# Kernel tuning notes

Measured on AMD Instinct MI355X. Metric: run time of the kernel, lower is better.

The kernel has to match this reference:

```python
import jax, jax.numpy as jnp
import numpy as np

N, E, D, H, C = 50000, 800000, 256, 8, 32  # C = D // H
STEPS = 6
NEG = 0.2  # leaky_relu negative slope (PyG HEATConv default)
ETD, EAD = 10, 50  # edge_type_emb_dim, edge_attr_emb_dim


def setup_inputs() -> dict:
    key = jax.random.key(0)
    ks = jax.random.split(key, 20)
    def g(k, shape, scale=0.05):
        return jax.random.normal(k, shape, dtype=jnp.float32) * scale
    return {
        "x": jax.random.normal(ks[0], (N, D), dtype=jnp.float32),
        "edge_index": jax.random.randint(ks[1], (2, E), 0, N),
        "edge_attr": jax.random.normal(ks[2], (E,), dtype=jnp.float32),
        "node_type": jax.random.randint(ks[3], (N,), 0, 2),
        "link_type": jax.random.randint(ks[4], (E,), 0, 3),
        # HEATConv params (shared across all 6 steps)
        "Wh": g(ks[5], (2, D, C)),          # HeteroLinear weight per node type
        "bh": g(ks[6], (2, C)),             # HeteroLinear bias per node type
        "Et": g(ks[7], (3, ETD)),           # edge type embedding table
        "Wea": g(ks[8], (1, EAD)),          # edge attr embedding (Linear, no bias)
        "Watt": g(ks[9], (2 * C + ETD + EAD, H)),  # attention (Linear, no bias)
        "Wlin": g(ks[10], (C + EAD, C)),    # message lin (Linear, no bias)
        # per-step FFN + LayerNorm params
        "ffn_w1": g(ks[11], (STEPS, D, 4 * D)),
        "ffn_b1": g(ks[12], (STEPS, 4 * D)),
        "ffn_w2": g(ks[13], (STEPS, 4 * D, D)),
        "ffn_b2": g(ks[14], (STEPS, D)),
        "ln1_g": jnp.ones((STEPS, D), jnp.float32),
        "ln1_b": jnp.zeros((STEPS, D), jnp.float32),
        "ln2_g": jnp.ones((STEPS, D), jnp.float32),
        "ln2_b": jnp.zeros((STEPS, D), jnp.float32),
    }


def _leaky(v):
    return jax.nn.leaky_relu(v, NEG)


def _layer_norm(h, g, b, eps=1e-5):
    mu = h.mean(-1, keepdims=True)
    var = h.var(-1, keepdims=True)  # biased, matches torch LayerNorm
    return (h - mu) * jax.lax.rsqrt(var + eps) * g + b


def _heat_conv(m, src, dst, edge_attr, node_type, link_type, Wh, bh, Et, Wea, Watt, Wlin):
    # node-type-specific linear (HeteroLinear, 2 types): compute both, select
    x_all = jnp.einsum('nd,tdc->tnc', m, Wh) + bh[:, None, :]     # [2,N,C]
    x = jnp.where(node_type[:, None] == 0, x_all[0], x_all[1])    # [N,C]
    ete = _leaky(Et[link_type])                                   # [E,ETD]
    eae = _leaky(edge_attr[:, None] @ Wea)                        # [E,EAD]
    feat = jnp.concatenate([x[dst], x[src], ete, eae], axis=-1)   # [E, 2C+ETD+EAD]
    logits = _leaky(feat @ Watt)                                  # [E,H]
    # segment softmax over incoming edges of each destination node
    mx = jax.ops.segment_max(logits, dst, num_segments=N)
    e = jnp.exp(logits - mx[dst])
    s = jax.ops.segment_sum(e, dst, num_segments=N)
    alpha = e / (s[dst] + 1e-16)                                  # [E,H]
    msg = jnp.concatenate([x[src], eae], axis=-1) @ Wlin          # [E,C]
    per_edge = alpha[:, :, None] * msg[:, None, :]                # [E,H,C]
    out = jax.ops.segment_sum(per_edge, dst, num_segments=N)      # [N,H,C]
    return out.reshape(N, H * C)  # concat heads; root_weight=False


def reference(x, edge_index, edge_attr, node_type, link_type, Wh, bh, Et, Wea, Watt, Wlin,
              ffn_w1, ffn_b1, ffn_w2, ffn_b2, ln1_g, ln1_b, ln2_g, ln2_b):
    src, dst = edge_index[0], edge_index[1]
    m = x
    for i in range(STEPS):
        h = _heat_conv(m, src, dst, edge_attr, node_type, link_type,
                       Wh, bh, Et, Wea, Watt, Wlin)
        m = _layer_norm(h + m, ln1_g[i], ln1_b[i])
        f = jax.nn.relu(m @ ffn_w1[i] + ffn_b1[i]) @ ffn_w2[i] + ffn_b2[i]
        m = _layer_norm(f + m, ln2_g[i], ln2_b[i])
    return m
```

## Files before the change

kernel.cpp:

```cpp
#include <hip/hip_runtime.h>

#define Nn 50000
#define Ee 800000
#define STEPSn 6
#define NP 49

typedef _Float16 half8 __attribute__((ext_vector_type(8)));
typedef _Float16 half4v __attribute__((ext_vector_type(4)));
typedef float floatx4 __attribute__((ext_vector_type(4)));

typedef __attribute__((address_space(1))) void gvoid_t;
typedef __attribute__((address_space(3))) void svoid_t;

__device__ __forceinline__ float leakyf(float v) { return v > 0.f ? v : 0.2f * v; }

__device__ __forceinline__ void gload16(const void* g, void* l) {
    __builtin_amdgcn_global_load_lds((const gvoid_t*)g, (svoid_t*)l, 16, 0, 0);
}

template <int CTRL>
__device__ __forceinline__ float dppf(float v) {
    return __int_as_float(__builtin_amdgcn_update_dpp(
        0, __float_as_int(v), CTRL, 0xF, 0xF, true));
}

__global__ void k_count(const int* __restrict__ dst, int* __restrict__ cnt) {
    int e = blockIdx.x * 256 + threadIdx.x;
    if (e < Ee) atomicAdd(&cnt[dst[e]], 1);
}

__global__ __launch_bounds__(256) void k_scan1(const int* __restrict__ cnt,
                                               int* __restrict__ part) {
    int b = blockIdx.x, t = threadIdx.x;
    int s = 0;
#pragma unroll
    for (int j = 0; j < 4; ++j) {
        int idx = b * 1024 + j * 256 + t;
        if (idx < Nn) s += cnt[idx];
    }
#pragma unroll
    for (int d = 1; d < 64; d <<= 1) s += __shfl_xor(s, d);
    __shared__ int ws[4];
    if ((t & 63) == 0) ws[t >> 6] = s;
    __syncthreads();
    if (t == 0) part[b] = ws[0] + ws[1] + ws[2] + ws[3];
}

__global__ void k_scan2(const int* __restrict__ part, int* __restrict__ pref,
                        int* __restrict__ offN) {
    int t = threadIdx.x;
    int v = (t < NP) ? part[t] : 0;
    int p = v;
#pragma unroll
    for (int d = 1; d < 64; d <<= 1) {
        int u = __shfl_up(p, d);
        if (t >= d) p += u;
    }
    if (t < NP) pref[t] = p - v;
    if (t == 63) offN[0] = p;
}

__global__ __launch_bounds__(256) void k_scan3(const int* __restrict__ cnt,
                                               const int* __restrict__ pref,
                                               int* __restrict__ off) {
    __shared__ int wsum[4];
    int b = blockIdx.x, t = threadIdx.x;
    int base = b * 1024;
    int v[4];
    int s = 0;
#pragma unroll
    for (int j = 0; j < 4; ++j) {
        int idx = base + t * 4 + j;
        v[j] = (idx < Nn) ? cnt[idx] : 0;
        s += v[j];
    }
    int lane = t & 63, w = t >> 6;
    int ps = s;
#pragma unroll
    for (int d = 1; d < 64; d <<= 1) {
        int u = __shfl_up(ps, d);
        if (lane >= d) ps += u;
    }
    if (lane == 63) wsum[w] = ps;
    __syncthreads();
    int woff = 0;
    for (int i = 0; i < w; ++i) woff += wsum[i];
    int ex = pref[b] + woff + ps - s;
#pragma unroll
    for (int j = 0; j < 4; ++j) {
        int idx = base + t * 4 + j;
        if (idx < Nn) off[idx] = ex;
        ex += v[j];
    }
}

__global__ void k_fill(const int* __restrict__ src, const int* __restrict__ dst,
                       const float* __restrict__ edge_attr, const int* __restrict__ link_type,
                       const int* __restrict__ off, int* __restrict__ cur,
                       int2* __restrict__ edata) {
    int e = blockIdx.x * 256 + threadIdx.x;
    if (e >= Ee) return;
    int d = dst[e];
    int slot = off[d] + atomicAdd(&cur[d], 1);
    edata[slot] = make_int2(src[e] | (link_type[e] << 20), __float_as_int(edge_attr[e]));
}

__global__ void k_const(const float* __restrict__ Et, const float* __restrict__ Wea,
                        const float* __restrict__ Watt, const float* __restrict__ Wlin,
                        float* __restrict__ C) {
    __shared__ float u[50], v[50];
    int t = threadIdx.x;
    if (t < 50) {
        float w = Wea[t];
        u[t] = w * (w > 0.f ? 1.f : 0.2f);
        v[t] = w * (w < 0.f ? 1.f : 0.2f);
    }
    __syncthreads();
    if (t < 8) {
        float a = 0.f, b = 0.f;
        for (int j = 0; j < 50; ++j) {
            float w = Watt[(74 + j) * 8 + t];
            a += u[j] * w;
            b += v[j] * w;
        }
        C[t] = a;
        C[8 + t] = b;
    } else if (t < 32) {
        int lt = (t - 8) >> 3, h = (t - 8) & 7;
        float a = 0.f;
        for (int j = 0; j < 10; ++j) a += leakyf(Et[lt * 10 + j]) * Watt[(64 + j) * 8 + h];
        C[16 + (t - 8)] = a;
    } else if (t < 64) {
        int c = t - 32;
        float a = 0.f, b = 0.f;
        for (int j = 0; j < 50; ++j) {
            float w = Wlin[(32 + j) * 32 + c];
            a += u[j] * w;
            b += v[j] * w;
        }
        C[40 + c] = a;
        C[72 + c] = b;
    }
}

__global__ void k_comb(const float* __restrict__ Wh, const float* __restrict__ bh,
                       const float* __restrict__ Watt, const float* __restrict__ Wlin,
                       _Float16* __restrict__ Wcmb, float* __restrict__ bcmb) {
    int n = blockIdx.x;
    int k = threadIdx.x;
    if (n >= 96) {
        Wcmb[n * 256 + k] = (_Float16)0.f;
        return;
    }
    int ty = n / 48, c = n % 48;
    float a = 0.f;
    for (int kk = 0; kk < 32; ++kk) {
        float wsel;
        if (c < 32) wsel = Wlin[kk * 32 + c];
        else if (c < 40) wsel = Watt[kk * 8 + (c - 32)];
        else wsel = Watt[(32 + kk) * 8 + (c - 40)];
        a += Wh[ty * 8192 + k * 32 + kk] * wsel;
    }
    Wcmb[n * 256 + k] = (_Float16)a;
    if (k == 0) {
        float b = 0.f;
        for (int kk = 0; kk < 32; ++kk) {
            float wsel;
            if (c < 32) wsel = Wlin[kk * 32 + c];
            else if (c < 40) wsel = Watt[kk * 8 + (c - 32)];
            else wsel = Watt[(32 + kk) * 8 + (c - 40)];
            b += bh[ty * 32 + kk] * wsel;
        }
        bcmb[n] = b;
    }
}

__global__ void k_cvt(const float* __restrict__ x, _Float16* __restrict__ mh) {
    long i = ((long)blockIdx.x * 256 + threadIdx.x) * 4;
    if (i < (long)Nn * 256) {
        float4 v = *(const float4*)(x + i);
        half4v h;
        h[0] = (_Float16)v.x; h[1] = (_Float16)v.y;
        h[2] = (_Float16)v.z; h[3] = (_Float16)v.w;
        *(half4v*)(mh + i) = h;
    }
}

__global__ __launch_bounds__(256) void k_wtrans(const float* __restrict__ W,
                                                _Float16* __restrict__ WT,
                                                int K, int NN) {
    __shared__ float tile[64][65];
    int nk = K >> 6, nn = NN >> 6;
    int b = blockIdx.x;
    int s = b / (nk * nn);
    int r = b % (nk * nn);
    int kt = r / nn, nt = r % nn;
    const float* Ws = W + (long)s * K * NN;
    _Float16* WTs = WT + (long)s * K * NN;
    int lrow = threadIdx.x >> 6, lcol = threadIdx.x & 63;
#pragma unroll
    for (int i = 0; i < 16; ++i) {
        int row = i * 4 + lrow;
        tile[row][lcol] = Ws[(long)(kt * 64 + row) * NN + nt * 64 + lcol];
    }
    __syncthreads();
#pragma unroll
    for (int i = 0; i < 16; ++i) {
        int row = i * 4 + lrow;
        WTs[(long)(nt * 64 + row) * K + kt * 64 + lcol] = (_Float16)tile[lcol][row];
    }
}

__global__ __launch_bounds__(256) void k_node_proj2(
    const _Float16* __restrict__ mh, const int* __restrict__ node_type,
    const _Float16* __restrict__ Wcmb, const float* __restrict__ bcmb,
    float* __restrict__ adst, float* __restrict__ asrc,
    _Float16* __restrict__ xlin, int M) {
    __shared__ _Float16 sA[128 * 64];
    __shared__ _Float16 sB[128 * 64];
    __shared__ float sEpi[128][100];
    const int rowBase = blockIdx.x * 128;
    const int tid = threadIdx.x, wid = tid >> 6, lane = tid & 63;
    const int wm = (wid >> 1) * 64, wn = (wid & 1) * 64;

    floatx4 acc[4][4];
    floatx4 zz = {0.f, 0.f, 0.f, 0.f};
#pragma unroll
    for (int i = 0; i < 4; ++i)
#pragma unroll
        for (int j = 0; j < 4; ++j) acc[i][j] = zz;

    for (int k0 = 0; k0 < 256; k0 += 64) {
#pragma unroll
        for (int it = 0; it < 4; ++it) {
            int Ci = it * 256 + tid;
            int row = Ci >> 3, ch = Ci & 7;
            int gr = rowBase + row;
            if (gr > M - 1) gr = M - 1;
            gload16(mh + (long)gr * 256 + k0 + ((ch ^ (row & 7)) * 8),
                    &sA[(it * 256 + wid * 64) * 8]);
        }
#pragma unroll
        for (int it = 0; it < 4; ++it) {
            int Ci = it * 256 + tid;
            int row = Ci >> 3, ch = Ci & 7;
            gload16(Wcmb + (long)row * 256 + k0 + ((ch ^ (row & 7)) * 8),
                    &sB[(it * 256 + wid * 64) * 8]);
        }
        __syncthreads();
#pragma unroll
        for (int kk = 0; kk < 2; ++kk) {
            half8 af[4], bf[4];
#pragma unroll
            for (int i = 0; i < 4; ++i) {
                int row = wm + i * 16 + (lane & 15);
                int ch = (kk * 4 + (lane >> 4)) ^ (row & 7);
                af[i] = *(const half8*)&sA[row * 64 + ch * 8];
            }
#pragma unroll
            for (int j = 0; j < 4; ++j) {
                int row = wn + j * 16 + (lane & 15);
                int ch = (kk * 4 + (lane >> 4)) ^ (row & 7);
                bf[j] = *(const half8*)&sB[row * 64 + ch * 8];
            }
#pragma unroll
            for (int i = 0; i < 4; ++i)
#pragma unroll
                for (int j = 0; j < 4; ++j)
                    acc[i][j] = __builtin_amdgcn_mfma_f32_16x16x32_f16(af[i], bf[j], acc[i][j], 0, 0, 0);
        }
        __syncthreads();
    }
#pragma unroll
    for (int i = 0; i < 4; ++i)
#pragma unroll
        for (int j = 0; j < 4; ++j) {
            int col = wn + j * 16 + (lane & 15);
            if (col < 96) {
#pragma unroll
                for (int q = 0; q < 4; ++q)
                    sEpi[wm + i * 16 + (lane >> 4) * 4 + q][col] = acc[i][j][q];
            }
        }
    __syncthreads();
    for (int idx = tid; idx < 128 * 32; idx += 256) {
        int r = idx >> 5, c = idx & 31;
        int gr = rowBase + r;
        if (gr < M) {
            int ty = (node_type[gr] != 0) ? 1 : 0;
            int sc = ty * 48 + c;
            xlin[(long)gr * 32 + c] = (_Float16)(sEpi[r][sc] + bcmb[sc]);
        }
    }
    for (int idx = tid; idx < 128 * 8; idx += 256) {
        int r = idx >> 3, hh = idx & 7;
        int gr = rowBase + r;
        if (gr < M) {
            int ty = (node_type[gr] != 0) ? 1 : 0;
            adst[(long)gr * 8 + hh] = sEpi[r][ty * 48 + 32 + hh] + bcmb[ty * 48 + 32 + hh];
            asrc[(long)gr * 8 + hh] = sEpi[r][ty * 48 + 40 + hh] + bcmb[ty * 48 + 40 + hh];
        }
    }
}

__global__ __launch_bounds__(256) void k_edge_ln1(
    const int* __restrict__ off, const int2* __restrict__ edata,
    const float* __restrict__ C,
    const float* __restrict__ adst, const float* __restrict__ asrc,
    const _Float16* __restrict__ xlin, const _Float16* __restrict__ mres,
    const float* __restrict__ g1, const float* __restrict__ b1,
    _Float16* __restrict__ m1h) {
    __shared__ float sC[104];
    if (threadIdx.x < 104) sC[threadIdx.x] = C[threadIdx.x];
    __syncthreads();
    int n = blockIdx.x * 4 + (threadIdx.x >> 6);
    int lane = threadIdx.x & 63;
    long base = off[n];
    int deg = off[n + 1] - (int)base;
    int h = lane & 7;
    int hv = lane >> 5, lc = lane & 31;
    float adst_h = adst[(long)n * 8 + h];
    float linP = sC[40 + lc], linM = sC[72 + lc];
    float ssum = 0.f;
    float acc[8] = {0.f, 0.f, 0.f, 0.f, 0.f, 0.f, 0.f, 0.f};
    int deg2 = (deg + 1) & ~1;
    int i2 = hv;
    int2 edA = make_int2(0, 0);
    float asA = 0.f, xlA = 0.f;
    if (i2 < deg2) {
        long ei = base + (i2 < deg ? i2 : deg - 1);
        edA = edata[ei];
        int sA = edA.x & 0xFFFFF;
        asA = asrc[(long)sA * 8 + h];
        xlA = (float)xlin[(long)sA * 32 + lc];
    }
    while (i2 < deg2) {
        int i2n = i2 + 2;
        int2 edB = make_int2(0, 0);
        float asB = 0.f, xlB = 0.f;
        if (i2n < deg2) {
            long ein = base + (i2n < deg ? i2n : deg - 1);
            edB = edata[ein];
            int sB = edB.x & 0xFFFFF;
            asB = asrc[(long)sB * 8 + h];
            xlB = (float)xlin[(long)sB * 32 + lc];
        }
        bool valid = i2 < deg;
        int lt = edA.x >> 20;
        float t = __int_as_float(edA.y);
        float attc = sC[16 + lt * 8 + h] + t * (t > 0.f ? sC[h] : sC[8 + h]);
        float lg = adst_h + asA + attc;
        float w = valid ? __expf(leakyf(lg)) : 0.f;
        float msg = xlA + t * (t > 0.f ? linP : linM);
        if (lc < 8) ssum += w;
        float w4 = dppf<0x124>(w);
        acc[0] += dppf<0x00>(w) * msg;
        acc[1] += dppf<0x55>(w) * msg;
        acc[2] += dppf<0xAA>(w) * msg;
        acc[3] += dppf<0xFF>(w) * msg;
        acc[4] += dppf<0x00>(w4) * msg;
        acc[5] += dppf<0x55>(w4) * msg;
        acc[6] += dppf<0xAA>(w4) * msg;
        acc[7] += dppf<0xFF>(w4) * msg;
        edA = edB; asA = asB; xlA = xlB;
        i2 = i2n;
    }
    {
        bool sw = (lane & 4) != 0;
#pragma unroll
        for (int k = 0; k < 4; ++k) {
            float a = acc[k], b = acc[4 + k];
            acc[k] = sw ? b : a;
            acc[4 + k] = sw ? a : b;
        }
    }
#pragma unroll
    for (int hh = 0; hh < 8; ++hh) acc[hh] += __shfl_xor(acc[hh], 32);
    ssum += __shfl_xor(ssum, 32);
    float v[8];
    float s1 = 0.f, s2 = 0.f;
#pragma unroll
    for (int hh = 0; hh < 8; ++hh) {
        float sh = __shfl(ssum, hh);
        float o = acc[hh] / (sh + 1e-16f);
        float vv = o + (float)mres[(long)n * 256 + hh * 32 + lc];
        v[hh] = vv;
        s1 += vv;
        s2 += vv * vv;
    }
#pragma unroll
    for (int d = 1; d < 64; d <<= 1) { s1 += __shfl_xor(s1, d); s2 += __shfl_xor(s2, d); }
    float mu = s1 * (1.f / 512.f);
    float var = s2 * (1.f / 512.f) - mu * mu;
    float rs = rsqrtf(var + 1e-5f);
    if (hv == 0) {
#pragma unroll
        for (int hh = 0; hh < 8; ++hh) {
            int col = hh * 32 + lc;
            float o = (v[hh] - mu) * rs * g1[col] + b1[col];
            m1h[(long)n * 256 + col] = (_Float16)o;
        }
    }
}

#define HP 136
__global__ __launch_bounds__(512, 2) void k_ffn(
    const _Float16* __restrict__ A, const _Float16* __restrict__ W1,
    const float* __restrict__ b1, const _Float16* __restrict__ W2,
    const float* __restrict__ b2, const float* __restrict__ g2,
    const float* __restrict__ bln2, float* __restrict__ outp,
    _Float16* __restrict__ outh, int M, int writeOut) {
    __shared__ _Float16 sA[128 * 256];
    __shared__ _Float16 sH[128 * HP];
    __shared__ _Float16 sW[256 * 64];
    __shared__ float sS1[4][128], sS2[4][128];
    const int tid = threadIdx.x, wid = tid >> 6, lane = tid & 63;
    const int rowBase = blockIdx.x * 128;
    const int wtm = (wid >> 2) * 64;
    const int wtn1 = (wid & 3) * 32;
    const int wtn2 = (wid & 3) * 64;

#pragma unroll
    for (int it = 0; it < 8; ++it) {
        int Ci = it * 512 + tid;
        int row = Ci >> 5, c = Ci & 31;
        int gr = rowBase + row;
        if (gr > M - 1) gr = M - 1;
        int cs = (c & 24) | ((c & 7) ^ (row & 7));
        gload16(A + (long)gr * 256 + cs * 8, &sA[(it * 512 + wid * 64) * 8]);
    }

    floatx4 acc2[4][4];
    floatx4 zz = {0.f, 0.f, 0.f, 0.f};
#pragma unroll
    for (int i = 0; i < 4; ++i)
#pragma unroll
        for (int j = 0; j < 4; ++j) acc2[i][j] = zz;

    for (int ct = 0; ct < 8; ++ct) {
        floatx4 acc1[4][2];
#pragma unroll
        for (int i = 0; i < 4; ++i)
#pragma unroll
            for (int j = 0; j < 2; ++j) acc1[i][j] = zz;
        for (int ks = 0; ks < 4; ++ks) {
#pragma unroll
            for (int it = 0; it < 2; ++it) {
                int Ci = it * 512 + tid;
                int row = Ci >> 3, ch = Ci & 7;
                gload16(W1 + (long)(ct * 128 + row) * 256 + ks * 64 + ((ch ^ (row & 7)) * 8),
                        &sW[(it * 512 + wid * 64) * 8]);
            }
            __syncthreads();
#pragma unroll
            for (int kk = 0; kk < 2; ++kk) {
                half8 af[4], bf[2];
#pragma unroll
                for (int i = 0; i < 4; ++i) {
                    int row = wtm + i * 16 + (lane & 15);
                    int c = ks * 8 + kk * 4 + (lane >> 4);
                    int cs = (c & 24) | ((c & 7) ^ (row & 7));
                    af[i] = *(const half8*)&sA[row * 256 + cs * 8];
                }
#pragma unroll
                for (int j = 0; j < 2; ++j) {
                    int row = wtn1 + j * 16 + (lane & 15);
                    int ch = (kk * 4 + (lane >> 4)) ^ (row & 7);
                    bf[j] = *(const half8*)&sW[(row * 8 + ch) * 8];
                }
#pragma unroll
                for (int i = 0; i < 4; ++i)
#pragma unroll
                    for (int j = 0; j < 2; ++j)
                        acc1[i][j] = __builtin_amdgcn_mfma_f32_16x16x32_f16(af[i], bf[j], acc1[i][j], 0, 0, 0);
            }
            __syncthreads();
        }
#pragma unroll
        for (int j = 0; j < 2; ++j) {
            int kl = wtn1 + j * 16 + (lane & 15);
            float bv = b1[ct * 128 + kl];
#pragma unroll
            for (int i = 0; i < 4; ++i)
#pragma unroll
                for (int q = 0; q < 4; ++q) {
                    int m = wtm + i * 16 + (lane >> 4) * 4 + q;
                    float vv = acc1[i][j][q] + bv;
                    sH[m * HP + kl] = (_Float16)(vv > 0.f ? vv : 0.f);
                }
        }
        for (int ks2 = 0; ks2 < 2; ++ks2) {
#pragma unroll
            for (int it = 0; it < 4; ++it) {
                int Ci = it * 512 + tid;
                int row = Ci >> 3, ch = Ci & 7;
                gload16(W2 + (long)row * 1024 + ct * 128 + ks2 * 64 + ((ch ^ (row & 7)) * 8),
                        &sW[(it * 512 + wid * 64) * 8]);
            }
            __syncthreads();
#pragma unroll
            for (int kk = 0; kk < 2; ++kk) {
                half8 af[4], bf[4];
#pragma unroll
                for (int i = 0; i < 4; ++i) {
                    int m = wtm + i * 16 + (lane & 15);
                    af[i] = *(const half8*)&sH[m * HP + ks2 * 64 + (kk * 4 + (lane >> 4)) * 8];
                }
#pragma unroll
                for (int j = 0; j < 4; ++j) {
                    int nc = wtn2 + j * 16 + (lane & 15);
                    int ch = (kk * 4 + (lane >> 4)) ^ (nc & 7);
                    bf[j] = *(const half8*)&sW[(nc * 8 + ch) * 8];
                }
#pragma unroll
                for (int i = 0; i < 4; ++i)
#pragma unroll
                    for (int j = 0; j < 4; ++j)
                        acc2[i][j] = __builtin_amdgcn_mfma_f32_16x16x32_f16(af[i], bf[j], acc2[i][j], 0, 0, 0);
            }
            __syncthreads();
        }
    }
    const int cg = wid & 3;
#pragma unroll
    for (int i = 0; i < 4; ++i) {
#pragma unroll
        for (int q = 0; q < 4; ++q) {
            int rl = wtm + i * 16 + (lane >> 4) * 4 + q;
            float s1 = 0.f, s2 = 0.f;
#pragma unroll
            for (int j = 0; j < 4; ++j) {
                int col = wtn2 + j * 16 + (lane & 15);
                int cs = col >> 3;
                int csw = (cs & 24) | ((cs & 7) ^ (rl & 7));
                float rv = (float)sA[rl * 256 + csw * 8 + (col & 7)];
                float vv = acc2[i][j][q] + b2[col] + rv;
                acc2[i][j][q] = vv;
                s1 += vv;
                s2 += vv * vv;
            }
#pragma unroll
            for (int d = 1; d < 16; d <<= 1) {
                s1 += __shfl_xor(s1, d);
                s2 += __shfl_xor(s2, d);
            }
            if ((lane & 15) == 0) {
                sS1[cg][rl] = s1;
                sS2[cg][rl] = s2;
            }
        }
    }
    __syncthreads();
#pragma unroll
    for (int i = 0; i < 4; ++i) {
#pragma unroll
        for (int q = 0; q < 4; ++q) {
            int rl = wtm + i * 16 + (lane >> 4) * 4 + q;
            long grow = rowBase + rl;
            if (grow < M) {
                float t1 = sS1[0][rl] + sS1[1][rl] + sS1[2][rl] + sS1[3][rl];
                float t2 = sS2[0][rl] + sS2[1][rl] + sS2[2][rl] + sS2[3][rl];
                float mu = t1 * (1.f / 256.f);
                float var = t2 * (1.f / 256.f) - mu * mu;
                float rs = rsqrtf(var + 1e-5f);
#pragma unroll
                for (int j = 0; j < 4; ++j) {
                    int col = wtn2 + j * 16 + (lane & 15);
                    float o = (acc2[i][j][q] - mu) * rs * g2[col] + bln2[col];
                    outh[grow * 256 + col] = (_Float16)o;
                    if (writeOut) outp[grow * 256 + col] = o;
                }
            }
        }
    }
}

__global__ void k_fail(float* out) {
    if (threadIdx.x == 0 && blockIdx.x == 0) out[0] = 2.0e6f;
}

extern "C" void kernel_launch(void* const* d_in, const int* in_sizes, int n_in,
                              void* d_out, int out_size, void* d_ws, size_t ws_size,
                              hipStream_t stream) {
    const float* x = (const float*)d_in[0];
    const int* ei = (const int*)d_in[1];
    const float* edge_attr = (const float*)d_in[2];
    const int* node_type = (const int*)d_in[3];
    const int* link_type = (const int*)d_in[4];
    const float* Wh = (const float*)d_in[5];
    const float* bh = (const float*)d_in[6];
    const float* Et = (const float*)d_in[7];
    const float* Wea = (const float*)d_in[8];
    const float* Watt = (const float*)d_in[9];
    const float* Wlin = (const float*)d_in[10];
    const float* ffn_w1 = (const float*)d_in[11];
    const float* ffn_b1 = (const float*)d_in[12];
    const float* ffn_w2 = (const float*)d_in[13];
    const float* ffn_b2 = (const float*)d_in[14];
    const float* ln1_g = (const float*)d_in[15];
    const float* ln1_b = (const float*)d_in[16];
    const float* ln2_g = (const float*)d_in[17];
    const float* ln2_b = (const float*)d_in[18];
    const int* srcp = ei;
    const int* dstp = ei + Ee;

    size_t o = 0;
    auto carve = [&](size_t bytes) -> void* {
        void* p = (char*)d_ws + o;
        o += (bytes + 255) & ~(size_t)255;
        return p;
    };
    _Float16* m1h = (_Float16*)carve((size_t)Nn * 256 * 2);
    _Float16* mh = (_Float16*)carve((size_t)Nn * 256 * 2);
    float* adst = (float*)carve((size_t)Nn * 8 * 4);
    float* asrc = (float*)carve((size_t)Nn * 8 * 4);
    _Float16* xlin = (_Float16*)carve((size_t)Nn * 32 * 2);
    int2* edata = (int2*)carve((size_t)Ee * 8);
    int* off = (int*)carve((size_t)(Nn + 1) * 4);
    int* cnt = (int*)carve((size_t)Nn * 4);
    int* cur = (int*)carve((size_t)Nn * 4);
    int* part = (int*)carve(64 * 4);
    int* pref = (int*)carve(64 * 4);
    _Float16* W1T = (_Float16*)carve((size_t)STEPSn * 256 * 1024 * 2);
    _Float16* W2T = (_Float16*)carve((size_t)STEPSn * 256 * 1024 * 2);
    _Float16* Wcmb = (_Float16*)carve(128 * 256 * 2);
    float* bcmb = (float*)carve(128 * 4);
    float* econst = (float*)carve(104 * 4);
    if (o > ws_size) {
        k_fail<<<1, 64, 0, stream>>>((float*)d_out);
        return;
    }

    hipMemsetAsync(cnt, 0, (size_t)Nn * 4, stream);
    hipMemsetAsync(cur, 0, (size_t)Nn * 4, stream);
    k_count<<<3125, 256, 0, stream>>>(dstp, cnt);
    k_scan1<<<NP, 256, 0, stream>>>(cnt, part);
    k_scan2<<<1, 64, 0, stream>>>(part, pref, off + Nn);
    k_scan3<<<NP, 256, 0, stream>>>(cnt, pref, off);
    k_fill<<<3125, 256, 0, stream>>>(srcp, dstp, edge_attr, link_type, off, cur, edata);
    k_const<<<1, 128, 0, stream>>>(Et, Wea, Watt, Wlin, econst);
    k_comb<<<128, 256, 0, stream>>>(Wh, bh, Watt, Wlin, Wcmb, bcmb);
    k_cvt<<<12500, 256, 0, stream>>>(x, mh);
    k_wtrans<<<STEPSn * 64, 256, 0, stream>>>(ffn_w1, W1T, 256, 1024);
    k_wtrans<<<STEPSn * 64, 256, 0, stream>>>(ffn_w2, W2T, 1024, 256);

    const int nRP = (Nn + 127) / 128;
    for (int s = 0; s < STEPSn; ++s) {
        k_node_proj2<<<nRP, 256, 0, stream>>>(mh, node_type, Wcmb, bcmb,
                                              adst, asrc, xlin, Nn);
        k_edge_ln1<<<Nn / 4, 256, 0, stream>>>(off, edata, econst, adst, asrc,
                                               xlin, mh, ln1_g + s * 256, ln1_b + s * 256,
                                               m1h);
        k_ffn<<<nRP, 512, 0, stream>>>(m1h, W1T + (size_t)s * 262144,
                                       ffn_b1 + s * 1024, W2T + (size_t)s * 262144,
                                       ffn_b2 + s * 256, ln2_g + s * 256, ln2_b + s * 256,
                                       (float*)d_out, mh, Nn,
                                       (s == STEPSn - 1) ? 1 : 0);
    }
}
```

Before: 1.395 ms.

## Stream A tiles per k-step in FFN kernel to shrink LDS and stage fp16 stores

The FFN kernel no longer keeps the full 128x256 activation tile in shared memory. It streams 128x64 A slices alongside each W1 slice and splits the W2 stage into two 128-column halves, which cuts LDS use so two 512-thread blocks can fit per CU as the launch bounds request. The residual is now read back from global memory in the epilogue. The fp16 output is staged through LDS so each row segment is written with a 16-byte vector store. The cost is reloading A eight times per block (once per ct iteration), more barriers, and a global residual read.

```diff
diff --git a/kernel.cpp b/kernel.cpp
--- a/kernel.cpp
+++ b/kernel.cpp
@@ -410,25 +410,14 @@
     const float* __restrict__ b2, const float* __restrict__ g2,
     const float* __restrict__ bln2, float* __restrict__ outp,
     _Float16* __restrict__ outh, int M, int writeOut) {
-    __shared__ _Float16 sA[128 * 256];
+    __shared__ _Float16 sA[128 * 64];
+    __shared__ _Float16 sW[128 * 64];
     __shared__ _Float16 sH[128 * HP];
-    __shared__ _Float16 sW[256 * 64];
     __shared__ float sS1[4][128], sS2[4][128];
     const int tid = threadIdx.x, wid = tid >> 6, lane = tid & 63;
     const int rowBase = blockIdx.x * 128;
     const int wtm = (wid >> 2) * 64;
-    const int wtn1 = (wid & 3) * 32;
-    const int wtn2 = (wid & 3) * 64;
-
-#pragma unroll
-    for (int it = 0; it < 8; ++it) {
-        int Ci = it * 512 + tid;
-        int row = Ci >> 5, c = Ci & 31;
-        int gr = rowBase + row;
-        if (gr > M - 1) gr = M - 1;
-        int cs = (c & 24) | ((c & 7) ^ (row & 7));
-        gload16(A + (long)gr * 256 + cs * 8, &sA[(it * 512 + wid * 64) * 8]);
-    }
+    const int cg = wid & 3;
 
     floatx4 acc2[4][4];
     floatx4 zz = {0.f, 0.f, 0.f, 0.f};
@@ -444,6 +433,15 @@
 #pragma unroll
             for (int j = 0; j < 2; ++j) acc1[i][j] = zz;
         for (int ks = 0; ks < 4; ++ks) {
+#pragma unroll
+            for (int it = 0; it < 2; ++it) {
+                int Ci = it * 512 + tid;
+                int row = Ci >> 3, ch = Ci & 7;
+                int gr = rowBase + row;
+                if (gr > M - 1) gr = M - 1;
+                gload16(A + (long)gr * 256 + ks * 64 + ((ch ^ (row & 7)) * 8),
+                        &sA[(it * 512 + wid * 64) * 8]);
+            }
 #pragma unroll
             for (int it = 0; it < 2; ++it) {
                 int Ci = it * 512 + tid;
@@ -458,15 +456,14 @@
 #pragma unroll
                 for (int i = 0; i < 4; ++i) {
                     int row = wtm + i * 16 + (lane & 15);
-                    int c = ks * 8 + kk * 4 + (lane >> 4);
-                    int cs = (c & 24) | ((c & 7) ^ (row & 7));
-                    af[i] = *(const half8*)&sA[row * 256 + cs * 8];
+                    int ch = (kk * 4 + (lane >> 4)) ^ (row & 7);
+                    af[i] = *(const half8*)&sA[row * 64 + ch * 8];
                 }
 #pragma unroll
                 for (int j = 0; j < 2; ++j) {
-                    int row = wtn1 + j * 16 + (lane & 15);
+                    int row = cg * 32 + j * 16 + (lane & 15);
                     int ch = (kk * 4 + (lane >> 4)) ^ (row & 7);
-                    bf[j] = *(const half8*)&sW[(row * 8 + ch) * 8];
+                    bf[j] = *(const half8*)&sW[row * 64 + ch * 8];
                 }
 #pragma unroll
                 for (int i = 0; i < 4; ++i)
@@ -478,7 +475,7 @@
         }
 #pragma unroll
         for (int j = 0; j < 2; ++j) {
-            int kl = wtn1 + j * 16 + (lane & 15);
+            int kl = cg * 32 + j * 16 + (lane & 15);
             float bv = b1[ct * 128 + kl];
 #pragma unroll
             for (int i = 0; i < 4; ++i)
@@ -491,53 +488,56 @@
         }
         for (int ks2 = 0; ks2 < 2; ++ks2) {
 #pragma unroll
-            for (int it = 0; it < 4; ++it) {
-                int Ci = it * 512 + tid;
-                int row = Ci >> 3, ch = Ci & 7;
-                gload16(W2 + (long)row * 1024 + ct * 128 + ks2 * 64 + ((ch ^ (row & 7)) * 8),
-                        &sW[(it * 512 + wid * 64) * 8]);
-            }
-            __syncthreads();
-#pragma unroll
-            for (int kk = 0; kk < 2; ++kk) {
-                half8 af[4], bf[4];
-#pragma unroll
-                for (int i = 0; i < 4; ++i) {
-                    int m = wtm + i * 16 + (lane & 15);
-                    af[i] = *(const half8*)&sH[m * HP + ks2 * 64 + (kk * 4 + (lane >> 4)) * 8];
+            for (int nh = 0; nh < 2; ++nh) {
+#pragma unroll
+                for (int it = 0; it < 2; ++it) {
+                    int Ci = it * 512 + tid;
+                    int row = Ci >> 3, ch = Ci & 7;
+                    gload16(W2 + (long)(nh * 128 + row) * 1024 + ct * 128 + ks2 * 64 +
+                                ((ch ^ (row & 7)) * 8),
+                            &sW[(it * 512 + wid * 64) * 8]);
                 }
-#pragma unroll
-                for (int j = 0; j < 4; ++j) {
-                    int nc = wtn2 + j * 16 + (lane & 15);
-                    int ch = (kk * 4 + (lane >> 4)) ^ (nc & 7);
-                    bf[j] = *(const half8*)&sW[(nc * 8 + ch) * 8];
+                __syncthreads();
+#pragma unroll
+                for (int kk = 0; kk < 2; ++kk) {
+                    half8 af[4], bf[2];
+#pragma unroll
+                    for (int i = 0; i < 4; ++i) {
+                        int m = wtm + i * 16 + (lane & 15);
+                        af[i] = *(const half8*)&sH[m * HP + ks2 * 64 + (kk * 4 + (lane >> 4)) * 8];
+                    }
+#pragma unroll
+                    for (int j = 0; j < 2; ++j) {
+                        int cl = cg * 32 + j * 16 + (lane & 15);
+                        int ch = (kk * 4 + (lane >> 4)) ^ (cl & 7);
+                        bf[j] = *(const half8*)&sW[cl * 64 + ch * 8];
+                    }
+#pragma unroll
+                    for (int i = 0; i < 4; ++i)
+#pragma unroll
+                        for (int j = 0; j < 2; ++j)
+                            acc2[i][nh * 2 + j] = __builtin_amdgcn_mfma_f32_16x16x32_f16(
+                                af[i], bf[j], acc2[i][nh * 2 + j], 0, 0, 0);
                 }
-#pragma unroll
-                for (int i = 0; i < 4; ++i)
-#pragma unroll
-                    for (int j = 0; j < 4; ++j)
-                        acc2[i][j] = __builtin_amdgcn_mfma_f32_16x16x32_f16(af[i], bf[j], acc2[i][j], 0, 0, 0);
-            }
-            __syncthreads();
-        }
-    }
-    const int cg = wid & 3;
+                __syncthreads();
+            }
+        }
+    }
 #pragma unroll
     for (int i = 0; i < 4; ++i) {
 #pragma unroll
         for (int q = 0; q < 4; ++q) {
             int rl = wtm + i * 16 + (lane >> 4) * 4 + q;
+            long grow = rowBase + rl;
+            long gr = grow > M - 1 ? M - 1 : grow;
             float s1 = 0.f, s2 = 0.f;
 #pragma unroll
-            for (int j = 0; j < 4; ++j) {
-                int col = wtn2 + j * 16 + (lane & 15);
-                int cs = col >> 3;
-                int csw = (cs & 24) | ((cs & 7) ^ (rl & 7));
-                float rv = (float)sA[rl * 256 + csw * 8 + (col & 7)];
-                float vv = acc2[i][j][q] + b2[col] + rv;
-                acc2[i][j][q] = vv;
-                s1 += vv;
-                s2 += vv * vv;
+            for (int jj = 0; jj < 4; ++jj) {
+                int col = (jj >> 1) * 128 + cg * 32 + (jj & 1) * 16 + (lane & 15);
+                float v = acc2[i][jj][q] + b2[col] + (float)A[gr * 256 + col];
+                acc2[i][jj][q] = v;
+                s1 += v;
+                s2 += v * v;
             }
 #pragma unroll
             for (int d = 1; d < 16; d <<= 1) {
@@ -551,27 +551,37 @@
         }
     }
     __syncthreads();
+    _Float16* stg = &sW[wid * 1024];
 #pragma unroll
     for (int i = 0; i < 4; ++i) {
 #pragma unroll
         for (int q = 0; q < 4; ++q) {
             int rl = wtm + i * 16 + (lane >> 4) * 4 + q;
             long grow = rowBase + rl;
-            if (grow < M) {
-                float t1 = sS1[0][rl] + sS1[1][rl] + sS1[2][rl] + sS1[3][rl];
-                float t2 = sS2[0][rl] + sS2[1][rl] + sS2[2][rl] + sS2[3][rl];
-                float mu = t1 * (1.f / 256.f);
-                float var = t2 * (1.f / 256.f) - mu * mu;
-                float rs = rsqrtf(var + 1e-5f);
-#pragma unroll
-                for (int j = 0; j < 4; ++j) {
-                    int col = wtn2 + j * 16 + (lane & 15);
-                    float o = (acc2[i][j][q] - mu) * rs * g2[col] + bln2[col];
-                    outh[grow * 256 + col] = (_Float16)o;
-                    if (writeOut) outp[grow * 256 + col] = o;
-                }
-            }
-        }
+            float t1 = sS1[0][rl] + sS1[1][rl] + sS1[2][rl] + sS1[3][rl];
+            float t2 = sS2[0][rl] + sS2[1][rl] + sS2[2][rl] + sS2[3][rl];
+            float mu = t1 * (1.f / 256.f);
+            float var = t2 * (1.f / 256.f) - mu * mu;
+            float rs = rsqrtf(var + 1e-5f);
+#pragma unroll
+            for (int jj = 0; jj < 4; ++jj) {
+                int col = (jj >> 1) * 128 + cg * 32 + (jj & 1) * 16 + (lane & 15);
+                float o = (acc2[i][jj][q] - mu) * rs * g2[col] + bln2[col];
+                stg[((lane >> 4) * 4 + q) * 64 + jj * 16 + (lane & 15)] = (_Float16)o;
+                if (writeOut && grow < M) outp[grow * 256 + col] = o;
+            }
+        }
+        __asm__ volatile("s_waitcnt lgkmcnt(0)");
+#pragma unroll
+        for (int ps = 0; ps < 2; ++ps) {
+            int rloc = ps * 8 + (lane >> 3);
+            int p = (lane & 7) * 8;
+            half8 hv = *(const half8*)&stg[rloc * 64 + p];
+            long grow = rowBase + wtm + i * 16 + rloc;
+            int col = (p >> 5) * 128 + cg * 32 + (p & 16) + (p & 8);
+            if (grow < M) *(half8*)&outh[grow * 256 + col] = hv;
+        }
+        __asm__ volatile("s_waitcnt lgkmcnt(0)");
     }
 }
 
```

After: 1.484 ms. 6.4% more time.
